# Kernel tuning notes

Hardware: AMD Instinct MI355X
Metric: run time of the kernel (lower is better)

## Reference

```python
import jax, jax.numpy as jnp
import numpy as np
import math

# AAMsoftmax constants (m=0.2, s=30), matching the torch implementation
M = 0.2
S = 30.0
COS_M = math.cos(M)
SIN_M = math.sin(M)
TH = math.cos(math.pi - M)
MM = math.sin(math.pi - M) * M

B, IN, P, C = 4096, 1024, 256, 5994


def _l2norm(v):
    # F.normalize: v / max(||v||, eps)
    n = jnp.sqrt(jnp.sum(v * v, axis=-1, keepdims=True))
    return v / jnp.maximum(n, 1e-12)


def setup_inputs() -> dict:
    key = jax.random.key(0)
    k0, k1, k2, k3 = jax.random.split(key, 4)
    return {
        "x": jax.random.normal(k0, (B, IN), jnp.float32),
        "label": jax.random.randint(k1, (B,), 0, C, dtype=jnp.int32),
        "W_fc": jax.random.normal(k2, (P, IN), jnp.float32) * (1.0 / np.sqrt(IN)),
        "b_fc": jnp.zeros((P,), jnp.float32),
        "W_aam": jax.random.normal(k3, (C, P), jnp.float32) * 0.05,
    }


def reference(x, label, W_fc, b_fc, W_aam):
    # fc layer: [B, IN] -> [B, P]
    e = x @ W_fc.T + b_fc
    # cosine similarity against class prototypes: [B, C]
    cosine = _l2norm(e) @ _l2norm(W_aam).T
    sine = jnp.sqrt(jnp.clip(1.0 - cosine * cosine, 0.0, 1.0))
    phi = cosine * COS_M - sine * SIN_M
    # easy-margin-off fallback: use cosine - mm where angle too large
    phi = jnp.where((cosine - TH) > 0, phi, cosine - MM)
    one_hot = jax.nn.one_hot(label, C, dtype=cosine.dtype)
    logits = (one_hot * phi + (1.0 - one_hot) * cosine) * S
    # cross-entropy (mean over batch)
    logp = jax.nn.log_softmax(logits, axis=-1)
    nll = -jnp.take_along_axis(logp, label[:, None].astype(jnp.int32), axis=1)[:, 0]
    return jnp.mean(nll)
```

## Files before the change

### kernel.cpp

```cpp
#include <hip/hip_runtime.h>
#include <math.h>

typedef __attribute__((ext_vector_type(8))) short bf16x8;
typedef __attribute__((ext_vector_type(4))) float f32x4;

#define AAM_COS_M 0.9800665778412416f
#define AAM_SIN_M 0.19866933079506122f
#define AAM_TH   (-0.9800665778412416f)
#define AAM_MM    0.03973386615901225f
#define C_CLS 5994

__device__ inline ushort f2bf(float f) {
    unsigned x = __float_as_uint(f);
    return (ushort)((x + 0x7fffu + ((x >> 16) & 1u)) >> 16);
}
__device__ inline float bflo(unsigned u) { return __uint_as_float(u << 16); }
__device__ inline float bfhi(unsigned u) { return __uint_as_float(u & 0xffff0000u); }

__device__ __forceinline__ void gload16(const void* g, void* lds) {
    __builtin_amdgcn_global_load_lds(
        (const __attribute__((address_space(1))) unsigned int*)g,
        (__attribute__((address_space(3))) unsigned int*)lds, 16, 0, 0);
}

__global__ __launch_bounds__(256) void prep(const float* __restrict__ x,
                                            const float* __restrict__ Wfc,
                                            const float* __restrict__ Waam,
                                            ushort* __restrict__ xb,
                                            ushort* __restrict__ wfcb,
                                            ushort* __restrict__ Wn) {
    const int b = blockIdx.x;
    if (b < 4352) {
        const float* s = (b < 4096) ? x : Wfc;
        ushort* d      = (b < 4096) ? xb : wfcb;
        int i = (b < 4096 ? b : b - 4096) * 256 + threadIdx.x;
        float4 v = ((const float4*)s)[i];
        ushort4 o;
        o.x = f2bf(v.x); o.y = f2bf(v.y); o.z = f2bf(v.z); o.w = f2bf(v.w);
        ((ushort4*)d)[i] = o;
    } else {
        const int wave = threadIdx.x >> 6, lane = threadIdx.x & 63;
        const int row = (b - 4352) * 4 + wave;
        ushort4 o;
        if (row < C_CLS) {
            float4 v = ((const float4*)&Waam[(size_t)row * 256])[lane];
            float ss = v.x * v.x + v.y * v.y + v.z * v.z + v.w * v.w;
#pragma unroll
            for (int m = 32; m >= 1; m >>= 1) ss += __shfl_xor(ss, m, 64);
            float sc = 1.f / fmaxf(sqrtf(ss), 1e-12f);
            o.x = f2bf(v.x * sc); o.y = f2bf(v.y * sc);
            o.z = f2bf(v.z * sc); o.w = f2bf(v.w * sc);
        } else {
            o.x = 0; o.y = 0; o.z = 0; o.w = 0;
        }
        ((ushort4*)&Wn[(size_t)row * 256])[lane] = o;
    }
}

__global__ __launch_bounds__(256) void fc_mfma(const ushort* __restrict__ A,
                                               const ushort* __restrict__ Bm,
                                               const float* __restrict__ bias,
                                               float* __restrict__ C) {
    __shared__ ushort As[64 * 32];
    __shared__ ushort Bs[64 * 32];
    const int tid = threadIdx.x, lane = tid & 63, w = tid >> 6;
    const int wr = w >> 1, wc = w & 1;
    const int lx = lane & 15, lg = lane >> 4;
    const int l4 = lane >> 2, c8 = (lane & 3) << 3;
    const int rb = blockIdx.x * 64, cb = blockIdx.y * 64;

    f32x4 zero = {0.f, 0.f, 0.f, 0.f};
    f32x4 acc[2][2];
#pragma unroll
    for (int i = 0; i < 2; ++i)
#pragma unroll
        for (int j = 0; j < 2; ++j) acc[i][j] = zero;

    for (int k0 = 0; k0 < 1024; k0 += 32) {
        gload16(&A[(size_t)(rb + w * 16 + l4) * 1024 + k0 + c8], &As[w * 512]);
        gload16(&Bm[(size_t)(cb + w * 16 + l4) * 1024 + k0 + c8], &Bs[w * 512]);
        __syncthreads();
        bf16x8 af[2], bv[2];
#pragma unroll
        for (int f = 0; f < 2; ++f) {
            af[f] = *(const bf16x8*)&As[(wr * 32 + f * 16 + lx) * 32 + lg * 8];
            bv[f] = *(const bf16x8*)&Bs[(wc * 32 + f * 16 + lx) * 32 + lg * 8];
        }
#pragma unroll
        for (int i = 0; i < 2; ++i)
#pragma unroll
            for (int j = 0; j < 2; ++j)
                acc[i][j] = __builtin_amdgcn_mfma_f32_16x16x32_bf16(af[i], bv[j], acc[i][j], 0, 0, 0);
        __syncthreads();
    }
#pragma unroll
    for (int j = 0; j < 2; ++j) {
        int col = cb + wc * 32 + j * 16 + lx;
        float bb = bias[col];
#pragma unroll
        for (int i = 0; i < 2; ++i) {
            int row0 = rb + wr * 32 + i * 16 + lg * 4;
#pragma unroll
            for (int r = 0; r < 4; ++r)
                C[(size_t)(row0 + r) * 256 + col] = acc[i][j][r] + bb;
        }
    }
}

__global__ __launch_bounds__(256) void rownorm_e(const float* __restrict__ E,
                                                 ushort* __restrict__ En) {
    const int wave = threadIdx.x >> 6, lane = threadIdx.x & 63;
    const int row = blockIdx.x * 4 + wave;
    float4 v = ((const float4*)&E[(size_t)row * 256])[lane];
    float ss = v.x * v.x + v.y * v.y + v.z * v.z + v.w * v.w;
#pragma unroll
    for (int m = 32; m >= 1; m >>= 1) ss += __shfl_xor(ss, m, 64);
    float sc = 1.f / fmaxf(sqrtf(ss), 1e-12f);
    ushort4 o;
    o.x = f2bf(v.x * sc); o.y = f2bf(v.y * sc); o.z = f2bf(v.z * sc); o.w = f2bf(v.w * sc);
    ((ushort4*)&En[(size_t)row * 256])[lane] = o;
}

__global__ __launch_bounds__(256, 2) void aam_mfma(const ushort* __restrict__ A,
                                                   const ushort* __restrict__ Bm,
                                                   float* __restrict__ ps) {
    __shared__ ushort As[2][128 * 64];
    __shared__ ushort Bs[2][128 * 64];
    const int tid = threadIdx.x, lane = tid & 63, w = tid >> 6;
    const int wr = w >> 1, wc = w & 1;
    const int lx = lane & 15, lg = lane >> 4;
    const int rb = blockIdx.x * 128;
    const int split = blockIdx.y;

    const int lrow = lane >> 3;
    const int gcol = ((lane & 7) ^ lrow) * 8;

    float srun[16];
#pragma unroll
    for (int idx = 0; idx < 16; ++idx) srun[idx] = 0.f;

    f32x4 zero = {0.f, 0.f, 0.f, 0.f};
    f32x4 acc[4][4];
#pragma unroll
    for (int i = 0; i < 4; ++i)
#pragma unroll
        for (int j = 0; j < 4; ++j) acc[i][j] = zero;

#define AAM_STAGE(buf, g) do {                                                  \
    int t_ = (g) >> 2, k0_ = ((g) & 3) * 64;                                    \
    int cb_ = split * 384 + t_ * 128;                                           \
    _Pragma("unroll")                                                           \
    for (int s_ = 0; s_ < 4; ++s_) {                                            \
        int r0_ = w * 32 + s_ * 8;                                              \
        gload16(&A[(size_t)(rb + r0_ + lrow) * 256 + k0_ + gcol],               \
                &As[buf][r0_ * 64]);                                            \
        gload16(&Bm[(size_t)(cb_ + r0_ + lrow) * 256 + k0_ + gcol],             \
                &Bs[buf][r0_ * 64]);                                            \
    } } while (0)

    int cur = 0;
    AAM_STAGE(0, 0);
    __syncthreads();

    for (int g = 0; g < 12; ++g) {
        if (g < 11) AAM_STAGE(cur ^ 1, g + 1);
#pragma unroll
        for (int kk = 0; kk < 2; ++kk) {
            bf16x8 af[4], bv[4];
#pragma unroll
            for (int f = 0; f < 4; ++f) {
                int ra = wr * 64 + f * 16 + lx;
                int ca = (lg + kk * 4) ^ (lx & 7);
                af[f] = *(const bf16x8*)&As[cur][ra * 64 + ca * 8];
                int rq = wc * 64 + f * 16 + lx;
                bv[f] = *(const bf16x8*)&Bs[cur][rq * 64 + ca * 8];
            }
#pragma unroll
            for (int i = 0; i < 4; ++i)
#pragma unroll
                for (int j = 0; j < 4; ++j)
                    acc[i][j] = __builtin_amdgcn_mfma_f32_16x16x32_bf16(af[i], bv[j], acc[i][j], 0, 0, 0);
        }
        if ((g & 3) == 3) {
            int cb_ = split * 384 + (g >> 2) * 128;
#pragma unroll
            for (int j = 0; j < 4; ++j) {
                int c = cb_ + wc * 64 + j * 16 + lx;
                if (c < C_CLS) {
#pragma unroll
                    for (int i = 0; i < 4; ++i)
#pragma unroll
                        for (int r = 0; r < 4; ++r)
                            srun[i * 4 + r] += __expf(30.f * acc[i][j][r] - 30.f);
                }
            }
#pragma unroll
            for (int i = 0; i < 4; ++i)
#pragma unroll
                for (int j = 0; j < 4; ++j) acc[i][j] = zero;
        }
        __syncthreads();
        cur ^= 1;
    }
#undef AAM_STAGE

#pragma unroll
    for (int idx = 0; idx < 16; ++idx) {
#pragma unroll
        for (int msk = 1; msk < 16; msk <<= 1)
            srun[idx] += __shfl_xor(srun[idx], msk, 64);
        if (lx == 0) {
            int row = rb + wr * 64 + (idx >> 2) * 16 + lg * 4 + (idx & 3);
            int part = split * 2 + wc;
            ps[part * 4096 + row] = srun[idx];
        }
    }
}

__global__ __launch_bounds__(256) void reduce_all(const float* __restrict__ ps,
                                                  const ushort* __restrict__ En,
                                                  const ushort* __restrict__ Wn,
                                                  const int* __restrict__ lab,
                                                  float* __restrict__ partial) {
    __shared__ float red[4];
    const int wave = threadIdx.x >> 6, lane = threadIdx.x & 63;
    const int gw = blockIdx.x * 4 + wave;
    float acc = 0.f;
#pragma unroll
    for (int r = 0; r < 4; ++r) {
        const int row = gw * 4 + r;
        const int l = lab[row];
        uint2 a = ((const uint2*)&En[(size_t)row * 256])[lane];
        uint2 b = ((const uint2*)&Wn[(size_t)l * 256])[lane];
        float sum = bflo(a.x) * bflo(b.x) + bfhi(a.x) * bfhi(b.x)
                  + bflo(a.y) * bflo(b.y) + bfhi(a.y) * bfhi(b.y);
#pragma unroll
        for (int m = 32; m >= 1; m >>= 1) sum += __shfl_xor(sum, m, 64);
        float cv = sum;

        float s = (lane < 32) ? ps[lane * 4096 + row] : 0.f;
#pragma unroll
        for (int msk = 1; msk <= 32; msk <<= 1) s += __shfl_xor(s, msk, 64);

        float sine = sqrtf(fmaxf(1.f - cv * cv, 0.f));
        float phi = cv * AAM_COS_M - sine * AAM_SIN_M;
        phi = ((cv - AAM_TH) > 0.f) ? phi : (cv - AAM_MM);
        float denom = s - __expf(30.f * cv - 30.f) + __expf(30.f * phi - 30.f);
        acc += 30.f + logf(denom) - 30.f * phi;
    }
    if (lane == 0) red[wave] = acc;
    __syncthreads();
    if (threadIdx.x == 0)
        partial[blockIdx.x] = red[0] + red[1] + red[2] + red[3];
}

__global__ __launch_bounds__(256) void final_reduce(const float* __restrict__ partial,
                                                    float* __restrict__ out) {
    __shared__ float red[4];
    const int wave = threadIdx.x >> 6, lane = threadIdx.x & 63;
    float v = partial[threadIdx.x];
#pragma unroll
    for (int m = 32; m >= 1; m >>= 1) v += __shfl_xor(v, m, 64);
    if (lane == 0) red[wave] = v;
    __syncthreads();
    if (threadIdx.x == 0)
        out[0] = (red[0] + red[1] + red[2] + red[3]) * (1.f / 4096.f);
}

extern "C" void kernel_launch(void* const* d_in, const int* in_sizes, int n_in,
                              void* d_out, int out_size, void* d_ws, size_t ws_size,
                              hipStream_t stream) {
    const float* x    = (const float*)d_in[0];
    const int*   lab  = (const int*)d_in[1];
    const float* Wfc  = (const float*)d_in[2];
    const float* bfc  = (const float*)d_in[3];
    const float* Waam = (const float*)d_in[4];
    float* out = (float*)d_out;

    char* ws = (char*)d_ws;
    ushort* xb   = (ushort*)(ws);
    ushort* Wfcb = (ushort*)(ws + 8388608);
    float*  E    = (float*) (ws + 8912896);
    ushort* En   = (ushort*)(ws);
    ushort* Wn   = (ushort*)(ws + 13107200);
    float*  ps   = (float*) (ws + 16252928);
    float*  part = (float*) (ws + 16777216);

    prep<<<5888, 256, 0, stream>>>(x, Wfc, Waam, xb, Wfcb, Wn);
    fc_mfma<<<dim3(64, 4), 256, 0, stream>>>(xb, Wfcb, bfc, E);
    rownorm_e<<<1024, 256, 0, stream>>>(E, En);
    aam_mfma<<<dim3(32, 16), 256, 0, stream>>>(En, Wn, ps);
    reduce_all<<<256, 256, 0, stream>>>(ps, En, Wn, lab, part);
    final_reduce<<<1, 256, 0, stream>>>(part, out);
}
```

Before: 119.9 us.

## Capture label cosine inside AAM GEMM epilogue and simplify NLL reduction

The AAM GEMM epilogue now compares each column against the row's label and writes the label cosine directly. This removes the separate gather-and-dot of normalized embedding and prototype rows in the reduction kernel. The partial-sum layout becomes row-major so a thread-per-row reduction can read 32 partials with vector loads, and the final reduce shrinks to one wave. The cost is extra label loads and compares in the GEMM epilogue, plus more register pressure from the label array, on a kernel limited to 2 blocks per SM.

```diff
diff --git a/kernel.cpp b/kernel.cpp
--- a/kernel.cpp
+++ b/kernel.cpp
@@ -123,7 +123,9 @@
 
 __global__ __launch_bounds__(256, 2) void aam_mfma(const ushort* __restrict__ A,
                                                    const ushort* __restrict__ Bm,
-                                                   float* __restrict__ ps) {
+                                                   const int* __restrict__ lab,
+                                                   float* __restrict__ ps,
+                                                   float* __restrict__ cosl) {
     __shared__ ushort As[2][128 * 64];
     __shared__ ushort Bs[2][128 * 64];
     const int tid = threadIdx.x, lane = tid & 63, w = tid >> 6;
@@ -134,6 +136,11 @@
 
     const int lrow = lane >> 3;
     const int gcol = ((lane & 7) ^ lrow) * 8;
+
+    int labs[16];
+#pragma unroll
+    for (int idx = 0; idx < 16; ++idx)
+        labs[idx] = lab[rb + wr * 64 + (idx >> 2) * 16 + lg * 4 + (idx & 3)];
 
     float srun[16];
 #pragma unroll
@@ -190,8 +197,13 @@
 #pragma unroll
                     for (int i = 0; i < 4; ++i)
 #pragma unroll
-                        for (int r = 0; r < 4; ++r)
-                            srun[i * 4 + r] += __expf(30.f * acc[i][j][r] - 30.f);
+                        for (int r = 0; r < 4; ++r) {
+                            int idx = i * 4 + r;
+                            float cosv = acc[i][j][r];
+                            srun[idx] += __expf(30.f * cosv - 30.f);
+                            if (c == labs[idx])
+                                cosl[rb + wr * 64 + i * 16 + lg * 4 + r] = cosv;
+                        }
                 }
             }
 #pragma unroll
@@ -211,60 +223,44 @@
             srun[idx] += __shfl_xor(srun[idx], msk, 64);
         if (lx == 0) {
             int row = rb + wr * 64 + (idx >> 2) * 16 + lg * 4 + (idx & 3);
-            int part = split * 2 + wc;
-            ps[part * 4096 + row] = srun[idx];
-        }
-    }
-}
-
-__global__ __launch_bounds__(256) void reduce_all(const float* __restrict__ ps,
-                                                  const ushort* __restrict__ En,
-                                                  const ushort* __restrict__ Wn,
-                                                  const int* __restrict__ lab,
+            ps[(size_t)row * 32 + split * 2 + wc] = srun[idx];
+        }
+    }
+}
+
+__global__ __launch_bounds__(256) void reduce_nll(const float* __restrict__ ps,
+                                                  const float* __restrict__ cosl,
                                                   float* __restrict__ partial) {
     __shared__ float red[4];
+    const int row = blockIdx.x * 256 + threadIdx.x;
     const int wave = threadIdx.x >> 6, lane = threadIdx.x & 63;
-    const int gw = blockIdx.x * 4 + wave;
-    float acc = 0.f;
-#pragma unroll
-    for (int r = 0; r < 4; ++r) {
-        const int row = gw * 4 + r;
-        const int l = lab[row];
-        uint2 a = ((const uint2*)&En[(size_t)row * 256])[lane];
-        uint2 b = ((const uint2*)&Wn[(size_t)l * 256])[lane];
-        float sum = bflo(a.x) * bflo(b.x) + bfhi(a.x) * bfhi(b.x)
-                  + bflo(a.y) * bflo(b.y) + bfhi(a.y) * bfhi(b.y);
-#pragma unroll
-        for (int m = 32; m >= 1; m >>= 1) sum += __shfl_xor(sum, m, 64);
-        float cv = sum;
-
-        float s = (lane < 32) ? ps[lane * 4096 + row] : 0.f;
-#pragma unroll
-        for (int msk = 1; msk <= 32; msk <<= 1) s += __shfl_xor(s, msk, 64);
-
-        float sine = sqrtf(fmaxf(1.f - cv * cv, 0.f));
-        float phi = cv * AAM_COS_M - sine * AAM_SIN_M;
-        phi = ((cv - AAM_TH) > 0.f) ? phi : (cv - AAM_MM);
-        float denom = s - __expf(30.f * cv - 30.f) + __expf(30.f * phi - 30.f);
-        acc += 30.f + logf(denom) - 30.f * phi;
-    }
-    if (lane == 0) red[wave] = acc;
+    float s = 0.f;
+#pragma unroll
+    for (int q = 0; q < 8; ++q) {
+        float4 v = ((const float4*)&ps[(size_t)row * 32])[q];
+        s += v.x + v.y + v.z + v.w;
+    }
+    float cv = cosl[row];
+    float sine = sqrtf(fmaxf(1.f - cv * cv, 0.f));
+    float phi = cv * AAM_COS_M - sine * AAM_SIN_M;
+    phi = ((cv - AAM_TH) > 0.f) ? phi : (cv - AAM_MM);
+    float denom = s - __expf(30.f * cv - 30.f) + __expf(30.f * phi - 30.f);
+    float nll = 30.f + logf(denom) - 30.f * phi;
+#pragma unroll
+    for (int m = 32; m >= 1; m >>= 1) nll += __shfl_xor(nll, m, 64);
+    if (lane == 0) red[wave] = nll;
     __syncthreads();
     if (threadIdx.x == 0)
         partial[blockIdx.x] = red[0] + red[1] + red[2] + red[3];
 }
 
-__global__ __launch_bounds__(256) void final_reduce(const float* __restrict__ partial,
-                                                    float* __restrict__ out) {
-    __shared__ float red[4];
-    const int wave = threadIdx.x >> 6, lane = threadIdx.x & 63;
-    float v = partial[threadIdx.x];
+__global__ __launch_bounds__(64) void final_reduce(const float* __restrict__ partial,
+                                                   float* __restrict__ out) {
+    const int lane = threadIdx.x;
+    float v = (lane < 16) ? partial[lane] : 0.f;
 #pragma unroll
     for (int m = 32; m >= 1; m >>= 1) v += __shfl_xor(v, m, 64);
-    if (lane == 0) red[wave] = v;
-    __syncthreads();
-    if (threadIdx.x == 0)
-        out[0] = (red[0] + red[1] + red[2] + red[3]) * (1.f / 4096.f);
+    if (lane == 0) out[0] = v * (1.f / 4096.f);
 }
 
 extern "C" void kernel_launch(void* const* d_in, const int* in_sizes, int n_in,
@@ -284,12 +280,13 @@
     ushort* En   = (ushort*)(ws);
     ushort* Wn   = (ushort*)(ws + 13107200);
     float*  ps   = (float*) (ws + 16252928);
-    float*  part = (float*) (ws + 16777216);
+    float*  cosl = (float*) (ws + 16777216);
+    float*  part = (float*) (ws + 16793600);
 
     prep<<<5888, 256, 0, stream>>>(x, Wfc, Waam, xb, Wfcb, Wn);
     fc_mfma<<<dim3(64, 4), 256, 0, stream>>>(xb, Wfcb, bfc, E);
     rownorm_e<<<1024, 256, 0, stream>>>(E, En);
-    aam_mfma<<<dim3(32, 16), 256, 0, stream>>>(En, Wn, ps);
-    reduce_all<<<256, 256, 0, stream>>>(ps, En, Wn, lab, part);
-    final_reduce<<<1, 256, 0, stream>>>(part, out);
-}
+    aam_mfma<<<dim3(32, 16), 256, 0, stream>>>(En, Wn, lab, ps, cosl);
+    reduce_nll<<<16, 256, 0, stream>>>(ps, cosl, part);
+    final_reduce<<<1, 64, 0, stream>>>(part, out);
+}
```

Result: no change. 120.3 us (+0.3%).
